# Performance work log

Hardware: AMD Instinct MI355X
Metric: run time of the kernel (lower is better)

## Reference

```python
import jax, jax.numpy as jnp
import numpy as np

ALPHA = 0.1
STEPS = 4


def setup_inputs() -> dict:
    key = jax.random.key(0)
    x = jax.random.normal(key, (4, 8192, 1024), dtype=jnp.float32)
    return {"x": x}


def reference(x) -> jnp.ndarray:
    # CtaPostAttnMixer.forward, layout='bld', prefill, steps=4, alpha=0.1
    # Fixed-boundary 1D heat-diffusion stencil along the sequence dim.
    if x.shape[1] < 3:
        return x
    y = x.astype(jnp.float32)
    for _ in range(STEPS):
        # Laplacian on interior tokens: y[l+1] - 2 y[l] + y[l-1]
        lap = y[:, 2:, :] - 2.0 * y[:, 1:-1, :] + y[:, :-2, :]
        y = jnp.concatenate(
            [y[:, :1, :], y[:, 1:-1, :] + ALPHA * lap, y[:, -1:, :]], axis=1
        )
    return y.astype(x.dtype)
```

## Files before the change

kernel.cpp:

```cpp
#include <hip/hip_runtime.h>


namespace {

constexpr int Lr   = 8192;
constexpr int Dq   = 1024 / 4;
constexpr int Bn   = 4;
constexpr int C    = 16;
constexpr int H    = 8;
constexpr int SEG  = 64;
constexpr int SEGS = Lr / SEG;

constexpr float WK0 = 0.4870f;
constexpr float WK1 = 0.2144f;
constexpr float WK2 = 0.0388f;
constexpr float WK3 = 0.0032f;
constexpr float WK4 = 0.0001f;

__device__ __forceinline__ float4 f4_add(float4 a, float4 b) {
    return make_float4(a.x + b.x, a.y + b.y, a.z + b.z, a.w + b.w);
}
__device__ __forceinline__ float4 f4_mul(float s, float4 a) {
    return make_float4(s * a.x, s * a.y, s * a.z, s * a.w);
}
__device__ __forceinline__ float4 f4_fma(float s, float4 a, float4 c) {
    return make_float4(fmaf(s, a.x, c.x), fmaf(s, a.y, c.y),
                       fmaf(s, a.z, c.z), fmaf(s, a.w, c.w));
}

__global__ __launch_bounds__(256)
void mixer4_kernel(const float4* __restrict__ x, float4* __restrict__ y) {
    const int d4  = threadIdx.x;
    const int seg = blockIdx.x;
    const int b   = blockIdx.y;
    const int c_base = seg * SEG;

    const float4* __restrict__ xb = x + (size_t)b * Lr * Dq + d4;
    float4* __restrict__       yb = y + (size_t)b * Lr * Dq + d4;

    float4 w[C + H];

#pragma unroll
    for (int i = 0; i < C + H; ++i) {
        int gl = c_base - 4 + i;
        gl = gl < 0 ? 0 : gl;
        gl = gl > Lr - 1 ? Lr - 1 : gl;
        w[i] = xb[(size_t)gl * Dq];
    }

#pragma unroll
    for (int chunk = 0; chunk < SEG / C; ++chunk) {
        const int c0 = c_base + chunk * C;

        if (chunk > 0) {
#pragma unroll
            for (int i = 0; i < H; ++i) w[i] = w[C + i];
#pragma unroll
            for (int i = H; i < C + H; ++i) {
                int gl = c0 - 4 + i;
                gl = gl > Lr - 1 ? Lr - 1 : gl;
                w[i] = xb[(size_t)gl * Dq];
            }
        }

#pragma unroll
        for (int j = 0; j < C; ++j) {
            float4 acc = f4_mul(WK0, w[j + 4]);
            acc = f4_fma(WK1, f4_add(w[j + 3], w[j + 5]), acc);
            acc = f4_fma(WK2, f4_add(w[j + 2], w[j + 6]), acc);
            acc = f4_fma(WK3, f4_add(w[j + 1], w[j + 7]), acc);
            acc = f4_fma(WK4, f4_add(w[j + 0], w[j + 8]), acc);
            yb[(size_t)(c0 + j) * Dq] = acc;
        }

        if (c0 == 0) {
            yb[0] = w[4];
            {
                float4 o = f4_mul(0.2986f, w[4]);
                o = f4_fma(0.4482f, w[5], o);
                o = f4_fma(0.2112f, w[6], o);
                o = f4_fma(0.0387f, w[7], o);
                o = f4_fma(0.0032f, w[8], o);
                o = f4_fma(0.0001f, w[9], o);
                yb[(size_t)1 * Dq] = o;
            }
            {
                float4 o = f4_mul(0.0454f, w[4]);
                o = f4_fma(0.2112f, w[5], o);
                o = f4_fma(0.4869f, w[6], o);
                o = f4_fma(0.2144f, w[7], o);
                o = f4_fma(0.0388f, w[8], o);
                o = f4_fma(0.0032f, w[9], o);
                o = f4_fma(0.0001f, w[10], o);
                yb[(size_t)2 * Dq] = o;
            }
            {
                float4 o = f4_mul(0.0034f, w[4]);
                o = f4_fma(0.0387f, w[5], o);
                o = f4_fma(0.2144f, w[6], o);
                o = f4_fma(0.4870f, w[7], o);
                o = f4_fma(0.2144f, w[8], o);
                o = f4_fma(0.0388f, w[9], o);
                o = f4_fma(0.0032f, w[10], o);
                o = f4_fma(0.0001f, w[11], o);
                yb[(size_t)3 * Dq] = o;
            }
        }
        if (c0 == Lr - C) {
            yb[(size_t)(Lr - 1) * Dq] = w[19];
            {
                float4 o = f4_mul(0.2986f, w[19]);
                o = f4_fma(0.4482f, w[18], o);
                o = f4_fma(0.2112f, w[17], o);
                o = f4_fma(0.0387f, w[16], o);
                o = f4_fma(0.0032f, w[15], o);
                o = f4_fma(0.0001f, w[14], o);
                yb[(size_t)(Lr - 2) * Dq] = o;
            }
            {
                float4 o = f4_mul(0.0454f, w[19]);
                o = f4_fma(0.2112f, w[18], o);
                o = f4_fma(0.4869f, w[17], o);
                o = f4_fma(0.2144f, w[16], o);
                o = f4_fma(0.0388f, w[15], o);
                o = f4_fma(0.0032f, w[14], o);
                o = f4_fma(0.0001f, w[13], o);
                yb[(size_t)(Lr - 3) * Dq] = o;
            }
            {
                float4 o = f4_mul(0.0034f, w[19]);
                o = f4_fma(0.0387f, w[18], o);
                o = f4_fma(0.2144f, w[17], o);
                o = f4_fma(0.4870f, w[16], o);
                o = f4_fma(0.2144f, w[15], o);
                o = f4_fma(0.0388f, w[14], o);
                o = f4_fma(0.0032f, w[13], o);
                o = f4_fma(0.0001f, w[12], o);
                yb[(size_t)(Lr - 4) * Dq] = o;
            }
        }
    }
}

}

extern "C" void kernel_launch(void* const* d_in, const int* in_sizes, int n_in,
                              void* d_out, int out_size, void* d_ws, size_t ws_size,
                              hipStream_t stream) {
    const float4* x = (const float4*)d_in[0];
    float4*       y = (float4*)d_out;

    dim3 grid(SEGS, Bn);
    dim3 block(256);
    hipLaunchKernelGGL(mixer4_kernel, grid, block, 0, stream, x, y);
}
```

Baseline: 235.1 us.

## Process one chunk per block and use nontemporal stores

```diff
diff --git a/kernel.cpp b/kernel.cpp
--- a/kernel.cpp
+++ b/kernel.cpp
@@ -8,14 +8,15 @@
 constexpr int Bn   = 4;
 constexpr int C    = 16;
 constexpr int H    = 8;
-constexpr int SEG  = 64;
-constexpr int SEGS = Lr / SEG;
+constexpr int SEGS = Lr / C;
 
 constexpr float WK0 = 0.4870f;
 constexpr float WK1 = 0.2144f;
 constexpr float WK2 = 0.0388f;
 constexpr float WK3 = 0.0032f;
 constexpr float WK4 = 0.0001f;
+
+typedef float nfloat4 __attribute__((ext_vector_type(4)));
 
 __device__ __forceinline__ float4 f4_add(float4 a, float4 b) {
     return make_float4(a.x + b.x, a.y + b.y, a.z + b.z, a.w + b.w);
@@ -27,13 +28,18 @@
     return make_float4(fmaf(s, a.x, c.x), fmaf(s, a.y, c.y),
                        fmaf(s, a.z, c.z), fmaf(s, a.w, c.w));
 }
+__device__ __forceinline__ void f4_store_nt(float4* p, float4 v) {
+    nfloat4 nv;
+    nv.x = v.x; nv.y = v.y; nv.z = v.z; nv.w = v.w;
+    __builtin_nontemporal_store(nv, (nfloat4*)p);
+}
 
 __global__ __launch_bounds__(256)
 void mixer4_kernel(const float4* __restrict__ x, float4* __restrict__ y) {
     const int d4  = threadIdx.x;
     const int seg = blockIdx.x;
     const int b   = blockIdx.y;
-    const int c_base = seg * SEG;
+    const int c0  = seg * C;
 
     const float4* __restrict__ xb = x + (size_t)b * Lr * Dq + d4;
     float4* __restrict__       yb = y + (size_t)b * Lr * Dq + d4;
@@ -42,102 +48,86 @@
 
 #pragma unroll
     for (int i = 0; i < C + H; ++i) {
-        int gl = c_base - 4 + i;
+        int gl = c0 - 4 + i;
         gl = gl < 0 ? 0 : gl;
         gl = gl > Lr - 1 ? Lr - 1 : gl;
         w[i] = xb[(size_t)gl * Dq];
     }
 
 #pragma unroll
-    for (int chunk = 0; chunk < SEG / C; ++chunk) {
-        const int c0 = c_base + chunk * C;
+    for (int j = 0; j < C; ++j) {
+        float4 acc = f4_mul(WK0, w[j + 4]);
+        acc = f4_fma(WK1, f4_add(w[j + 3], w[j + 5]), acc);
+        acc = f4_fma(WK2, f4_add(w[j + 2], w[j + 6]), acc);
+        acc = f4_fma(WK3, f4_add(w[j + 1], w[j + 7]), acc);
+        acc = f4_fma(WK4, f4_add(w[j + 0], w[j + 8]), acc);
+        f4_store_nt(&yb[(size_t)(c0 + j) * Dq], acc);
+    }
 
-        if (chunk > 0) {
-#pragma unroll
-            for (int i = 0; i < H; ++i) w[i] = w[C + i];
-#pragma unroll
-            for (int i = H; i < C + H; ++i) {
-                int gl = c0 - 4 + i;
-                gl = gl > Lr - 1 ? Lr - 1 : gl;
-                w[i] = xb[(size_t)gl * Dq];
-            }
+    if (c0 == 0) {
+        f4_store_nt(&yb[0], w[4]);
+        {
+            float4 o = f4_mul(0.2986f, w[4]);
+            o = f4_fma(0.4482f, w[5], o);
+            o = f4_fma(0.2112f, w[6], o);
+            o = f4_fma(0.0387f, w[7], o);
+            o = f4_fma(0.0032f, w[8], o);
+            o = f4_fma(0.0001f, w[9], o);
+            f4_store_nt(&yb[(size_t)1 * Dq], o);
         }
-
-#pragma unroll
-        for (int j = 0; j < C; ++j) {
-            float4 acc = f4_mul(WK0, w[j + 4]);
-            acc = f4_fma(WK1, f4_add(w[j + 3], w[j + 5]), acc);
-            acc = f4_fma(WK2, f4_add(w[j + 2], w[j + 6]), acc);
-            acc = f4_fma(WK3, f4_add(w[j + 1], w[j + 7]), acc);
-            acc = f4_fma(WK4, f4_add(w[j + 0], w[j + 8]), acc);
-            yb[(size_t)(c0 + j) * Dq] = acc;
+        {
+            float4 o = f4_mul(0.0454f, w[4]);
+            o = f4_fma(0.2112f, w[5], o);
+            o = f4_fma(0.4869f, w[6], o);
+            o = f4_fma(0.2144f, w[7], o);
+            o = f4_fma(0.0388f, w[8], o);
+            o = f4_fma(0.0032f, w[9], o);
+            o = f4_fma(0.0001f, w[10], o);
+            f4_store_nt(&yb[(size_t)2 * Dq], o);
         }
-
-        if (c0 == 0) {
-            yb[0] = w[4];
-            {
-                float4 o = f4_mul(0.2986f, w[4]);
-                o = f4_fma(0.4482f, w[5], o);
-                o = f4_fma(0.2112f, w[6], o);
-                o = f4_fma(0.0387f, w[7], o);
-                o = f4_fma(0.0032f, w[8], o);
-                o = f4_fma(0.0001f, w[9], o);
-                yb[(size_t)1 * Dq] = o;
-            }
-            {
-                float4 o = f4_mul(0.0454f, w[4]);
-                o = f4_fma(0.2112f, w[5], o);
-                o = f4_fma(0.4869f, w[6], o);
-                o = f4_fma(0.2144f, w[7], o);
-                o = f4_fma(0.0388f, w[8], o);
-                o = f4_fma(0.0032f, w[9], o);
-                o = f4_fma(0.0001f, w[10], o);
-                yb[(size_t)2 * Dq] = o;
-            }
-            {
-                float4 o = f4_mul(0.0034f, w[4]);
-                o = f4_fma(0.0387f, w[5], o);
-                o = f4_fma(0.2144f, w[6], o);
-                o = f4_fma(0.4870f, w[7], o);
-                o = f4_fma(0.2144f, w[8], o);
-                o = f4_fma(0.0388f, w[9], o);
-                o = f4_fma(0.0032f, w[10], o);
-                o = f4_fma(0.0001f, w[11], o);
-                yb[(size_t)3 * Dq] = o;
-            }
+        {
+            float4 o = f4_mul(0.0034f, w[4]);
+            o = f4_fma(0.0387f, w[5], o);
+            o = f4_fma(0.2144f, w[6], o);
+            o = f4_fma(0.4870f, w[7], o);
+            o = f4_fma(0.2144f, w[8], o);
+            o = f4_fma(0.0388f, w[9], o);
+            o = f4_fma(0.0032f, w[10], o);
+            o = f4_fma(0.0001f, w[11], o);
+            f4_store_nt(&yb[(size_t)3 * Dq], o);
         }
-        if (c0 == Lr - C) {
-            yb[(size_t)(Lr - 1) * Dq] = w[19];
-            {
-                float4 o = f4_mul(0.2986f, w[19]);
-                o = f4_fma(0.4482f, w[18], o);
-                o = f4_fma(0.2112f, w[17], o);
-                o = f4_fma(0.0387f, w[16], o);
-                o = f4_fma(0.0032f, w[15], o);
-                o = f4_fma(0.0001f, w[14], o);
-                yb[(size_t)(Lr - 2) * Dq] = o;
-            }
-            {
-                float4 o = f4_mul(0.0454f, w[19]);
-                o = f4_fma(0.2112f, w[18], o);
-                o = f4_fma(0.4869f, w[17], o);
-                o = f4_fma(0.2144f, w[16], o);
-                o = f4_fma(0.0388f, w[15], o);
-                o = f4_fma(0.0032f, w[14], o);
-                o = f4_fma(0.0001f, w[13], o);
-                yb[(size_t)(Lr - 3) * Dq] = o;
-            }
-            {
-                float4 o = f4_mul(0.0034f, w[19]);
-                o = f4_fma(0.0387f, w[18], o);
-                o = f4_fma(0.2144f, w[17], o);
-                o = f4_fma(0.4870f, w[16], o);
-                o = f4_fma(0.2144f, w[15], o);
-                o = f4_fma(0.0388f, w[14], o);
-                o = f4_fma(0.0032f, w[13], o);
-                o = f4_fma(0.0001f, w[12], o);
-                yb[(size_t)(Lr - 4) * Dq] = o;
-            }
+    }
+    if (c0 == Lr - C) {
+        f4_store_nt(&yb[(size_t)(Lr - 1) * Dq], w[19]);
+        {
+            float4 o = f4_mul(0.2986f, w[19]);
+            o = f4_fma(0.4482f, w[18], o);
+            o = f4_fma(0.2112f, w[17], o);
+            o = f4_fma(0.0387f, w[16], o);
+            o = f4_fma(0.0032f, w[15], o);
+            o = f4_fma(0.0001f, w[14], o);
+            f4_store_nt(&yb[(size_t)(Lr - 2) * Dq], o);
+        }
+        {
+            float4 o = f4_mul(0.0454f, w[19]);
+            o = f4_fma(0.2112f, w[18], o);
+            o = f4_fma(0.4869f, w[17], o);
+            o = f4_fma(0.2144f, w[16], o);
+            o = f4_fma(0.0388f, w[15], o);
+            o = f4_fma(0.0032f, w[14], o);
+            o = f4_fma(0.0001f, w[13], o);
+            f4_store_nt(&yb[(size_t)(Lr - 3) * Dq], o);
+        }
+        {
+            float4 o = f4_mul(0.0034f, w[19]);
+            o = f4_fma(0.0387f, w[18], o);
+            o = f4_fma(0.2144f, w[17], o);
+            o = f4_fma(0.4870f, w[16], o);
+            o = f4_fma(0.2144f, w[15], o);
+            o = f4_fma(0.0388f, w[14], o);
+            o = f4_fma(0.0032f, w[13], o);
+            o = f4_fma(0.0001f, w[12], o);
+            f4_store_nt(&yb[(size_t)(Lr - 4) * Dq], o);
         }
     }
 }
```

Result: no change. 234.9 us (-0.1%).
